# Kernel tuning notes

Measured on AMD Instinct MI355X. Metric: run time of the kernel, lower is better.

Reference implementation:

```python
import jax, jax.numpy as jnp
import numpy as np

N_NODES = 50000
N_EDGES = 800000
IN_FEATS = 128
OUT_FEATS = 128


def setup_inputs() -> dict:
    key = jax.random.key(0)
    k1, k2, k3, k4, k5 = jax.random.split(key, 5)
    feat = jax.random.normal(k1, (N_NODES, IN_FEATS), dtype=jnp.float32)
    src = jax.random.randint(k2, (N_EDGES,), 0, N_NODES, dtype=jnp.int64)
    dst = jax.random.randint(k3, (N_EDGES,), 0, N_NODES, dtype=jnp.int64)
    # Glorot uniform weight, zero bias (as in reset_parameters)
    limit = float(np.sqrt(6.0 / (IN_FEATS + OUT_FEATS)))
    weight = jax.random.uniform(k4, (IN_FEATS, OUT_FEATS), dtype=jnp.float32,
                                minval=-limit, maxval=limit)
    bias = jnp.zeros((OUT_FEATS,), dtype=jnp.float32)
    return {"feat": feat, "src": src, "dst": dst, "weight": weight, "bias": bias}


def reference(feat, src, dst, weight, bias):
    ones = jnp.ones(src.shape[0], dtype=feat.dtype)
    # out-degree normalization on source side
    deg_out = jnp.maximum(jax.ops.segment_sum(ones, src, num_segments=N_NODES), 1.0)
    h = feat * (deg_out ** -0.5)[:, None]  # [N, in]
    # in_feats <= out_feats: aggregate first, then matmul
    agg = jax.ops.segment_sum(h[src], dst, num_segments=N_NODES)  # SpMM: [N, in]
    rst = jnp.matmul(agg, weight)  # [N, out]
    # in-degree normalization on destination side
    deg_in = jnp.maximum(jax.ops.segment_sum(ones, dst, num_segments=N_NODES), 1.0)
    rst = rst * (deg_in ** -0.5)[:, None]
    rst = rst + bias
    return rst
```

## Files before the change

kernel.cpp:

```cpp
#include <hip/hip_runtime.h>

#define IN_F 128
#define HRH 4
#define HCD 64
#define HCS 32
#define HRB 16
#define HIST_RS 12544
#define BIN_RS 3136
#define LROW 68

typedef __attribute__((ext_vector_type(8))) short bf16x8;
typedef __attribute__((ext_vector_type(4))) float f32x4;

static __device__ __forceinline__ unsigned short f2bf(float x) {
    unsigned u = __float_as_uint(x);
    unsigned r = (u + 0x7FFFu + ((u >> 16) & 1u)) >> 16;
    return (unsigned short)r;
}

__global__ __launch_bounds__(256) void k_hist(const int* __restrict__ src,
                                              const int* __restrict__ dst,
                                              int* __restrict__ dstpart,
                                              int* __restrict__ srcpart,
                                              int nN, int nE) {
    __shared__ int h[HIST_RS];
    int bid = blockIdx.x;
    const int* key;
    int* part;
    int r, c, nch;
    if (bid < HRH * HCD) {
        key = dst; part = dstpart; nch = HCD;
        r = bid / HCD; c = bid % HCD;
    } else {
        bid -= HRH * HCD;
        key = src; part = srcpart; nch = HCS;
        r = bid / HCS; c = bid % HCS;
    }
    const int rs   = (nN + HRH - 1) / HRH;
    const int rbeg = r * rs;
    const int rsize = min(rs, nN - rbeg);
    if (rsize <= 0) return;

    for (int i = threadIdx.x; i < rsize; i += 256) h[i] = 0;
    __syncthreads();

    const int chunk = (nE + nch - 1) / nch;
    const int ebeg = c * chunk;
    const int eend = min(ebeg + chunk, nE);

    if ((ebeg & 3) == 0) {
        for (int i = ebeg + threadIdx.x * 4; i < eend; i += 256 * 4) {
            if (i + 3 < eend) {
                const int4 k4 = *reinterpret_cast<const int4*>(key + i);
                int a;
                a = k4.x - rbeg; if ((unsigned)a < (unsigned)rsize) atomicAdd(&h[a], 1);
                a = k4.y - rbeg; if ((unsigned)a < (unsigned)rsize) atomicAdd(&h[a], 1);
                a = k4.z - rbeg; if ((unsigned)a < (unsigned)rsize) atomicAdd(&h[a], 1);
                a = k4.w - rbeg; if ((unsigned)a < (unsigned)rsize) atomicAdd(&h[a], 1);
            } else {
                for (int j = i; j < eend; ++j) {
                    int a = key[j] - rbeg;
                    if ((unsigned)a < (unsigned)rsize) atomicAdd(&h[a], 1);
                }
            }
        }
    } else {
        for (int i = ebeg + threadIdx.x; i < eend; i += 256) {
            int a = key[i] - rbeg;
            if ((unsigned)a < (unsigned)rsize) atomicAdd(&h[a], 1);
        }
    }
    __syncthreads();

    int* pout = part + (size_t)c * nN + rbeg;
    for (int i = threadIdx.x; i < rsize; i += 256) pout[i] = h[i];
}

__global__ void k_merge(int* __restrict__ dstpart, const int* __restrict__ srcpart,
                        int* __restrict__ cnt_in,
                        float* __restrict__ dinv_out, float* __restrict__ dinv_in,
                        int nN) {
    const int n = blockIdx.x * blockDim.x + threadIdx.x;
    if (n >= nN) return;
    int s = 0;
#pragma unroll 4
    for (int c = 0; c < HCS; ++c) s += srcpart[(size_t)c * nN + n];
    int run = 0;
#pragma unroll 4
    for (int c = 0; c < HCD; ++c) {
        const size_t idx = (size_t)c * nN + n;
        int v = dstpart[idx];
        dstpart[idx] = run;
        run += v;
    }
    cnt_in[n]   = run;
    dinv_out[n] = rsqrtf(fmaxf((float)s, 1.0f));
    dinv_in[n]  = rsqrtf(fmaxf((float)run, 1.0f));
}

__global__ __launch_bounds__(256) void k_scan_blk(const int* __restrict__ cnt,
                                                  int* __restrict__ offs,
                                                  int* __restrict__ part, int nN) {
    __shared__ int ts[256];
    const int t = threadIdx.x;
    const int base = blockIdx.x * 1024 + t * 4;
    int4 v = make_int4(0, 0, 0, 0);
    if (base + 3 < nN) {
        v = *reinterpret_cast<const int4*>(cnt + base);
    } else {
        if (base + 0 < nN) v.x = cnt[base + 0];
        if (base + 1 < nN) v.y = cnt[base + 1];
        if (base + 2 < nN) v.z = cnt[base + 2];
        if (base + 3 < nN) v.w = cnt[base + 3];
    }
    const int s = v.x + v.y + v.z + v.w;
    ts[t] = s;
    __syncthreads();
    for (int d = 1; d < 256; d <<= 1) {
        int u = (t >= d) ? ts[t - d] : 0;
        __syncthreads();
        ts[t] += u;
        __syncthreads();
    }
    const int ex = ts[t] - s;
    if (t == 255) part[blockIdx.x] = ts[255];
    int4 o;
    o.x = ex;
    o.y = o.x + v.x;
    o.z = o.y + v.y;
    o.w = o.z + v.z;
    if (base + 3 < nN) {
        *reinterpret_cast<int4*>(offs + base) = o;
    } else {
        if (base + 0 < nN) offs[base + 0] = o.x;
        if (base + 1 < nN) offs[base + 1] = o.y;
        if (base + 2 < nN) offs[base + 2] = o.z;
        if (base + 3 < nN) offs[base + 3] = o.w;
    }
}

__global__ __launch_bounds__(256) void k_scan_top(int* __restrict__ part, int nb) {
    __shared__ int ts[256];
    const int t = threadIdx.x;
    const int v = (t < nb) ? part[t] : 0;
    ts[t] = v;
    __syncthreads();
    for (int d = 1; d < 256; d <<= 1) {
        int u = (t >= d) ? ts[t - d] : 0;
        __syncthreads();
        ts[t] += u;
        __syncthreads();
    }
    if (t < nb) part[t] = ts[t] - v;
}

__global__ __launch_bounds__(256) void k_scan_add(int* __restrict__ offs,
                                                  const int* __restrict__ part,
                                                  int nN, int nE) {
    const int base = blockIdx.x * 1024 + threadIdx.x * 4;
    const int add = part[blockIdx.x];
    if (base + 3 < nN) {
        int4 o = *reinterpret_cast<int4*>(offs + base);
        o.x += add; o.y += add; o.z += add; o.w += add;
        *reinterpret_cast<int4*>(offs + base) = o;
    } else {
#pragma unroll
        for (int j = 0; j < 4; ++j)
            if (base + j < nN) offs[base + j] += add;
    }
    if (blockIdx.x == 0 && threadIdx.x == 0) offs[nN] = nE;
}

__global__ __launch_bounds__(256) void k_bin2(const int* __restrict__ src,
                                              const int* __restrict__ dst,
                                              const int* __restrict__ offs,
                                              const int* __restrict__ chunkoff,
                                              int* __restrict__ eidx, int nN, int nE) {
    __shared__ int cur[BIN_RS];
    const int bid = blockIdx.x;
    const int r = bid / HCD;
    const int c = bid % HCD;
    const int rs = (nN + HRB - 1) / HRB;
    const int rbeg = r * rs;
    const int rsize = min(rs, nN - rbeg);
    if (rsize <= 0) return;

    for (int i = threadIdx.x; i < rsize; i += 256)
        cur[i] = offs[rbeg + i] + chunkoff[(size_t)c * nN + rbeg + i];
    __syncthreads();

    const int chunk = (nE + HCD - 1) / HCD;
    const int ebeg = c * chunk;
    const int eend = min(ebeg + chunk, nE);
    for (int i = ebeg + threadIdx.x * 4; i < eend; i += 256 * 4) {
        if (i + 3 < eend) {
            const int4 d4 = *reinterpret_cast<const int4*>(dst + i);
            int d;
            d = d4.x - rbeg; if ((unsigned)d < (unsigned)rsize) { int p = atomicAdd(&cur[d], 1); eidx[p] = src[i + 0]; }
            d = d4.y - rbeg; if ((unsigned)d < (unsigned)rsize) { int p = atomicAdd(&cur[d], 1); eidx[p] = src[i + 1]; }
            d = d4.z - rbeg; if ((unsigned)d < (unsigned)rsize) { int p = atomicAdd(&cur[d], 1); eidx[p] = src[i + 2]; }
            d = d4.w - rbeg; if ((unsigned)d < (unsigned)rsize) { int p = atomicAdd(&cur[d], 1); eidx[p] = src[i + 3]; }
        } else {
            for (int j = i; j < eend; ++j) {
                int d = dst[j] - rbeg;
                if ((unsigned)d < (unsigned)rsize) { int p = atomicAdd(&cur[d], 1); eidx[p] = src[j]; }
            }
        }
    }
}

__global__ __launch_bounds__(256) void k_scale(const float* __restrict__ feat,
                                               const float* __restrict__ dinv,
                                               unsigned short* __restrict__ h, int nN) {
    const int i = blockIdx.x * 256 + threadIdx.x;
    if (i >= nN * (IN_F / 4)) return;
    const int node = i >> 5;
    const int j = (i & 31) * 4;
    const float s = dinv[node];
    const float4 v = *reinterpret_cast<const float4*>(feat + (size_t)node * IN_F + j);
    ushort4 o;
    o.x = f2bf(v.x * s);
    o.y = f2bf(v.y * s);
    o.z = f2bf(v.z * s);
    o.w = f2bf(v.w * s);
    *reinterpret_cast<ushort4*>(h + (size_t)node * IN_F + j) = o;
}

__global__ __launch_bounds__(256) void k_wprep(const float* __restrict__ W,
                                               unsigned short* __restrict__ wt) {
    __shared__ float wl[128 * 128];
    for (int i = threadIdx.x * 4; i < 128 * 128; i += 256 * 4)
        *reinterpret_cast<float4*>(&wl[i]) = *reinterpret_cast<const float4*>(&W[i]);
    __syncthreads();
    const int col = threadIdx.x >> 1;
    const int k0  = (threadIdx.x & 1) * 64;
    for (int k = k0; k < k0 + 64; ++k)
        wt[col * 128 + k] = f2bf(wl[k * 128 + col]);
}

__global__ __launch_bounds__(256) void k_gg(
    const unsigned short* __restrict__ h, const int* __restrict__ eidx,
    const int* __restrict__ offs, const unsigned short* __restrict__ wt,
    const float* __restrict__ bias, const float* __restrict__ dinv_in,
    float* __restrict__ out, int nN) {
    __shared__ unsigned tile[16 * LROW];
    const int lane = threadIdx.x & 63;
    const int wave = threadIdx.x >> 6;
    const int blk16 = blockIdx.x * 16;
    const size_t lo = (size_t)(lane * 2);

    for (int j = 0; j < 4; ++j) {
        const int trow = wave * 4 + j;
        const int node = blk16 + trow;
        float ax = 0.0f, ay = 0.0f;
        if (node < nN) {
            const int beg = offs[node], end = offs[node + 1];
            int i = beg;
            for (; i + 8 <= end; i += 8) {
                const int s0 = eidx[i + 0], s1 = eidx[i + 1], s2 = eidx[i + 2], s3 = eidx[i + 3];
                const int s4 = eidx[i + 4], s5 = eidx[i + 5], s6 = eidx[i + 6], s7 = eidx[i + 7];
                const unsigned v0 = *reinterpret_cast<const unsigned*>(h + (size_t)s0 * IN_F + lo);
                const unsigned v1 = *reinterpret_cast<const unsigned*>(h + (size_t)s1 * IN_F + lo);
                const unsigned v2 = *reinterpret_cast<const unsigned*>(h + (size_t)s2 * IN_F + lo);
                const unsigned v3 = *reinterpret_cast<const unsigned*>(h + (size_t)s3 * IN_F + lo);
                const unsigned v4 = *reinterpret_cast<const unsigned*>(h + (size_t)s4 * IN_F + lo);
                const unsigned v5 = *reinterpret_cast<const unsigned*>(h + (size_t)s5 * IN_F + lo);
                const unsigned v6 = *reinterpret_cast<const unsigned*>(h + (size_t)s6 * IN_F + lo);
                const unsigned v7 = *reinterpret_cast<const unsigned*>(h + (size_t)s7 * IN_F + lo);
                ax += __uint_as_float(v0 << 16);          ay += __uint_as_float(v0 & 0xFFFF0000u);
                ax += __uint_as_float(v1 << 16);          ay += __uint_as_float(v1 & 0xFFFF0000u);
                ax += __uint_as_float(v2 << 16);          ay += __uint_as_float(v2 & 0xFFFF0000u);
                ax += __uint_as_float(v3 << 16);          ay += __uint_as_float(v3 & 0xFFFF0000u);
                ax += __uint_as_float(v4 << 16);          ay += __uint_as_float(v4 & 0xFFFF0000u);
                ax += __uint_as_float(v5 << 16);          ay += __uint_as_float(v5 & 0xFFFF0000u);
                ax += __uint_as_float(v6 << 16);          ay += __uint_as_float(v6 & 0xFFFF0000u);
                ax += __uint_as_float(v7 << 16);          ay += __uint_as_float(v7 & 0xFFFF0000u);
            }
            for (; i < end; ++i) {
                const int s = eidx[i];
                const unsigned v = *reinterpret_cast<const unsigned*>(h + (size_t)s * IN_F + lo);
                ax += __uint_as_float(v << 16);
                ay += __uint_as_float(v & 0xFFFF0000u);
            }
        }
        tile[trow * LROW + lane] = ((unsigned)f2bf(ay) << 16) | (unsigned)f2bf(ax);
    }
    __syncthreads();

    const int g = lane >> 4;
    const int cl = lane & 15;

    float di[4];
#pragma unroll
    for (int q = 0; q < 4; ++q)
        di[q] = dinv_in[min(blk16 + g * 4 + q, nN - 1)];

    f32x4 acc0 = (f32x4){0.f, 0.f, 0.f, 0.f};
    f32x4 acc1 = (f32x4){0.f, 0.f, 0.f, 0.f};
    const int col0 = wave * 16 + cl;
    const int col1 = (wave + 4) * 16 + cl;

#pragma unroll
    for (int s = 0; s < 4; ++s) {
        const bf16x8 a = *reinterpret_cast<const bf16x8*>(tile + cl * LROW + s * 16 + g * 4);
        const bf16x8 b0 = *reinterpret_cast<const bf16x8*>(wt + (size_t)col0 * IN_F + s * 32 + g * 8);
        const bf16x8 b1 = *reinterpret_cast<const bf16x8*>(wt + (size_t)col1 * IN_F + s * 32 + g * 8);
        acc0 = __builtin_amdgcn_mfma_f32_16x16x32_bf16(a, b0, acc0, 0, 0, 0);
        acc1 = __builtin_amdgcn_mfma_f32_16x16x32_bf16(a, b1, acc1, 0, 0, 0);
    }

    const float bv0 = bias[col0];
    const float bv1 = bias[col1];
#pragma unroll
    for (int q = 0; q < 4; ++q) {
        const int rr = blk16 + g * 4 + q;
        if (rr < nN) {
            out[(size_t)rr * IN_F + col0] = acc0[q] * di[q] + bv0;
            out[(size_t)rr * IN_F + col1] = acc1[q] * di[q] + bv1;
        }
    }
}

extern "C" void kernel_launch(void* const* d_in, const int* in_sizes, int n_in,
                              void* d_out, int out_size, void* d_ws, size_t ws_size,
                              hipStream_t stream) {
    const float* feat = (const float*)d_in[0];
    const int*   src  = (const int*)d_in[1];
    const int*   dst  = (const int*)d_in[2];
    const float* W    = (const float*)d_in[3];
    const float* bias = (const float*)d_in[4];
    float*       out  = (float*)d_out;

    const int nE = in_sizes[1];
    const int nN = in_sizes[0] / IN_F;
    const int nb = (nN + 1023) / 1024;

    char* base = (char*)d_ws;
    int*            dstpart  = (int*)base;
    int*            srcpart  = (int*)(base + (size_t)HCD * nN * 4);
    unsigned short* h        = (unsigned short*)base;
    int*            eidx     = (int*)(base + (size_t)HCD * nN * 4 + (size_t)nN * IN_F * 2);
    unsigned short* wt       = (unsigned short*)(eidx + nE);
    int*            cnt_in   = (int*)(wt + 128 * 128);
    float*          dinv_out = (float*)(cnt_in + nN);
    float*          dinv_in  = dinv_out + nN;
    int*            offs     = (int*)(dinv_in + nN);
    int*            partscan = offs + nN + 1;

    k_hist    <<<HRH * (HCD + HCS), 256, 0, stream>>>(src, dst, dstpart, srcpart, nN, nE);
    k_merge   <<<(nN + 255) / 256, 256, 0, stream>>>(dstpart, srcpart, cnt_in, dinv_out, dinv_in, nN);
    k_scan_blk<<<nb, 256, 0, stream>>>(cnt_in, offs, partscan, nN);
    k_scan_top<<<1, 256, 0, stream>>>(partscan, nb);
    k_scan_add<<<nb, 256, 0, stream>>>(offs, partscan, nN, nE);
    k_bin2    <<<HRB * HCD, 256, 0, stream>>>(src, dst, offs, dstpart, eidx, nN, nE);
    k_scale   <<<(nN * (IN_F / 4) + 255) / 256, 256, 0, stream>>>(feat, dinv_out, h, nN);
    k_wprep   <<<1, 256, 0, stream>>>(W, wt);
    k_gg      <<<(nN + 15) / 16, 256, 0, stream>>>(h, eidx, offs, wt, bias, dinv_in, out, nN);
}
```

Baseline: 132.4 us.

## Pad per-node edge lists to multiples of eight and halve bin row blocks

Measured after the change: 121.3 us. -8.4%, faster.

```diff
diff --git a/kernel.cpp b/kernel.cpp
--- a/kernel.cpp
+++ b/kernel.cpp
@@ -4,9 +4,9 @@
 #define HRH 4
 #define HCD 64
 #define HCS 32
-#define HRB 16
+#define HRB 8
 #define HIST_RS 12544
-#define BIN_RS 3136
+#define BIN_RS 6272
 #define LROW 68
 
 typedef __attribute__((ext_vector_type(8))) short bf16x8;
@@ -77,11 +77,12 @@
 }
 
 __global__ void k_merge(int* __restrict__ dstpart, const int* __restrict__ srcpart,
-                        int* __restrict__ cnt_in,
+                        int* __restrict__ cnt_pad, int* __restrict__ creal,
                         float* __restrict__ dinv_out, float* __restrict__ dinv_in,
                         int nN) {
     const int n = blockIdx.x * blockDim.x + threadIdx.x;
-    if (n >= nN) return;
+    if (n > nN) return;
+    if (n == nN) { cnt_pad[n] = 0; return; }
     int s = 0;
 #pragma unroll 4
     for (int c = 0; c < HCS; ++c) s += srcpart[(size_t)c * nN + n];
@@ -93,25 +94,26 @@
         dstpart[idx] = run;
         run += v;
     }
-    cnt_in[n]   = run;
+    cnt_pad[n]  = (run + 7) & ~7;
+    creal[n]    = run;
     dinv_out[n] = rsqrtf(fmaxf((float)s, 1.0f));
     dinv_in[n]  = rsqrtf(fmaxf((float)run, 1.0f));
 }
 
 __global__ __launch_bounds__(256) void k_scan_blk(const int* __restrict__ cnt,
                                                   int* __restrict__ offs,
-                                                  int* __restrict__ part, int nN) {
+                                                  int* __restrict__ part, int nNs) {
     __shared__ int ts[256];
     const int t = threadIdx.x;
     const int base = blockIdx.x * 1024 + t * 4;
     int4 v = make_int4(0, 0, 0, 0);
-    if (base + 3 < nN) {
+    if (base + 3 < nNs) {
         v = *reinterpret_cast<const int4*>(cnt + base);
     } else {
-        if (base + 0 < nN) v.x = cnt[base + 0];
-        if (base + 1 < nN) v.y = cnt[base + 1];
-        if (base + 2 < nN) v.z = cnt[base + 2];
-        if (base + 3 < nN) v.w = cnt[base + 3];
+        if (base + 0 < nNs) v.x = cnt[base + 0];
+        if (base + 1 < nNs) v.y = cnt[base + 1];
+        if (base + 2 < nNs) v.z = cnt[base + 2];
+        if (base + 3 < nNs) v.w = cnt[base + 3];
     }
     const int s = v.x + v.y + v.z + v.w;
     ts[t] = s;
@@ -129,13 +131,13 @@
     o.y = o.x + v.x;
     o.z = o.y + v.y;
     o.w = o.z + v.z;
-    if (base + 3 < nN) {
+    if (base + 3 < nNs) {
         *reinterpret_cast<int4*>(offs + base) = o;
     } else {
-        if (base + 0 < nN) offs[base + 0] = o.x;
-        if (base + 1 < nN) offs[base + 1] = o.y;
-        if (base + 2 < nN) offs[base + 2] = o.z;
-        if (base + 3 < nN) offs[base + 3] = o.w;
+        if (base + 0 < nNs) offs[base + 0] = o.x;
+        if (base + 1 < nNs) offs[base + 1] = o.y;
+        if (base + 2 < nNs) offs[base + 2] = o.z;
+        if (base + 3 < nNs) offs[base + 3] = o.w;
     }
 }
 
@@ -156,19 +158,27 @@
 
 __global__ __launch_bounds__(256) void k_scan_add(int* __restrict__ offs,
                                                   const int* __restrict__ part,
-                                                  int nN, int nE) {
+                                                  int nNs) {
     const int base = blockIdx.x * 1024 + threadIdx.x * 4;
     const int add = part[blockIdx.x];
-    if (base + 3 < nN) {
+    if (base + 3 < nNs) {
         int4 o = *reinterpret_cast<int4*>(offs + base);
         o.x += add; o.y += add; o.z += add; o.w += add;
         *reinterpret_cast<int4*>(offs + base) = o;
     } else {
 #pragma unroll
         for (int j = 0; j < 4; ++j)
-            if (base + j < nN) offs[base + j] += add;
-    }
-    if (blockIdx.x == 0 && threadIdx.x == 0) offs[nN] = nE;
+            if (base + j < nNs) offs[base + j] += add;
+    }
+}
+
+__global__ void k_pad(const int* __restrict__ offs, const int* __restrict__ creal,
+                      int* __restrict__ eidx, int nN) {
+    const int n = blockIdx.x * blockDim.x + threadIdx.x;
+    if (n >= nN) return;
+    const int s = offs[n] + creal[n];
+    const int e = offs[n + 1];
+    for (int i = s; i < e; ++i) eidx[i] = nN;
 }
 
 __global__ __launch_bounds__(256) void k_bin2(const int* __restrict__ src,
@@ -213,16 +223,18 @@
                                                const float* __restrict__ dinv,
                                                unsigned short* __restrict__ h, int nN) {
     const int i = blockIdx.x * 256 + threadIdx.x;
-    if (i >= nN * (IN_F / 4)) return;
+    if (i >= (nN + 1) * (IN_F / 4)) return;
     const int node = i >> 5;
     const int j = (i & 31) * 4;
-    const float s = dinv[node];
-    const float4 v = *reinterpret_cast<const float4*>(feat + (size_t)node * IN_F + j);
-    ushort4 o;
-    o.x = f2bf(v.x * s);
-    o.y = f2bf(v.y * s);
-    o.z = f2bf(v.z * s);
-    o.w = f2bf(v.w * s);
+    ushort4 o = make_ushort4(0, 0, 0, 0);
+    if (node < nN) {
+        const float s = dinv[node];
+        const float4 v = *reinterpret_cast<const float4*>(feat + (size_t)node * IN_F + j);
+        o.x = f2bf(v.x * s);
+        o.y = f2bf(v.y * s);
+        o.z = f2bf(v.z * s);
+        o.w = f2bf(v.w * s);
+    }
     *reinterpret_cast<ushort4*>(h + (size_t)node * IN_F + j) = o;
 }
 
@@ -255,32 +267,33 @@
         float ax = 0.0f, ay = 0.0f;
         if (node < nN) {
             const int beg = offs[node], end = offs[node + 1];
-            int i = beg;
-            for (; i + 8 <= end; i += 8) {
-                const int s0 = eidx[i + 0], s1 = eidx[i + 1], s2 = eidx[i + 2], s3 = eidx[i + 3];
-                const int s4 = eidx[i + 4], s5 = eidx[i + 5], s6 = eidx[i + 6], s7 = eidx[i + 7];
-                const unsigned v0 = *reinterpret_cast<const unsigned*>(h + (size_t)s0 * IN_F + lo);
-                const unsigned v1 = *reinterpret_cast<const unsigned*>(h + (size_t)s1 * IN_F + lo);
-                const unsigned v2 = *reinterpret_cast<const unsigned*>(h + (size_t)s2 * IN_F + lo);
-                const unsigned v3 = *reinterpret_cast<const unsigned*>(h + (size_t)s3 * IN_F + lo);
-                const unsigned v4 = *reinterpret_cast<const unsigned*>(h + (size_t)s4 * IN_F + lo);
-                const unsigned v5 = *reinterpret_cast<const unsigned*>(h + (size_t)s5 * IN_F + lo);
-                const unsigned v6 = *reinterpret_cast<const unsigned*>(h + (size_t)s6 * IN_F + lo);
-                const unsigned v7 = *reinterpret_cast<const unsigned*>(h + (size_t)s7 * IN_F + lo);
-                ax += __uint_as_float(v0 << 16);          ay += __uint_as_float(v0 & 0xFFFF0000u);
-                ax += __uint_as_float(v1 << 16);          ay += __uint_as_float(v1 & 0xFFFF0000u);
-                ax += __uint_as_float(v2 << 16);          ay += __uint_as_float(v2 & 0xFFFF0000u);
-                ax += __uint_as_float(v3 << 16);          ay += __uint_as_float(v3 & 0xFFFF0000u);
-                ax += __uint_as_float(v4 << 16);          ay += __uint_as_float(v4 & 0xFFFF0000u);
-                ax += __uint_as_float(v5 << 16);          ay += __uint_as_float(v5 & 0xFFFF0000u);
-                ax += __uint_as_float(v6 << 16);          ay += __uint_as_float(v6 & 0xFFFF0000u);
-                ax += __uint_as_float(v7 << 16);          ay += __uint_as_float(v7 & 0xFFFF0000u);
-            }
-            for (; i < end; ++i) {
-                const int s = eidx[i];
-                const unsigned v = *reinterpret_cast<const unsigned*>(h + (size_t)s * IN_F + lo);
-                ax += __uint_as_float(v << 16);
-                ay += __uint_as_float(v & 0xFFFF0000u);
+            if (beg < end) {
+                int4 ea = *reinterpret_cast<const int4*>(eidx + beg);
+                int4 eb = *reinterpret_cast<const int4*>(eidx + beg + 4);
+                for (int i = beg; i < end; i += 8) {
+                    const int s0 = ea.x, s1 = ea.y, s2 = ea.z, s3 = ea.w;
+                    const int s4 = eb.x, s5 = eb.y, s6 = eb.z, s7 = eb.w;
+                    const unsigned v0 = *reinterpret_cast<const unsigned*>(h + (size_t)s0 * IN_F + lo);
+                    const unsigned v1 = *reinterpret_cast<const unsigned*>(h + (size_t)s1 * IN_F + lo);
+                    const unsigned v2 = *reinterpret_cast<const unsigned*>(h + (size_t)s2 * IN_F + lo);
+                    const unsigned v3 = *reinterpret_cast<const unsigned*>(h + (size_t)s3 * IN_F + lo);
+                    const unsigned v4 = *reinterpret_cast<const unsigned*>(h + (size_t)s4 * IN_F + lo);
+                    const unsigned v5 = *reinterpret_cast<const unsigned*>(h + (size_t)s5 * IN_F + lo);
+                    const unsigned v6 = *reinterpret_cast<const unsigned*>(h + (size_t)s6 * IN_F + lo);
+                    const unsigned v7 = *reinterpret_cast<const unsigned*>(h + (size_t)s7 * IN_F + lo);
+                    if (i + 8 < end) {
+                        ea = *reinterpret_cast<const int4*>(eidx + i + 8);
+                        eb = *reinterpret_cast<const int4*>(eidx + i + 12);
+                    }
+                    ax += __uint_as_float(v0 << 16);          ay += __uint_as_float(v0 & 0xFFFF0000u);
+                    ax += __uint_as_float(v1 << 16);          ay += __uint_as_float(v1 & 0xFFFF0000u);
+                    ax += __uint_as_float(v2 << 16);          ay += __uint_as_float(v2 & 0xFFFF0000u);
+                    ax += __uint_as_float(v3 << 16);          ay += __uint_as_float(v3 & 0xFFFF0000u);
+                    ax += __uint_as_float(v4 << 16);          ay += __uint_as_float(v4 & 0xFFFF0000u);
+                    ax += __uint_as_float(v5 << 16);          ay += __uint_as_float(v5 & 0xFFFF0000u);
+                    ax += __uint_as_float(v6 << 16);          ay += __uint_as_float(v6 & 0xFFFF0000u);
+                    ax += __uint_as_float(v7 << 16);          ay += __uint_as_float(v7 & 0xFFFF0000u);
+                }
             }
         }
         tile[trow * LROW + lane] = ((unsigned)f2bf(ay) << 16) | (unsigned)f2bf(ax);
@@ -333,27 +346,31 @@
 
     const int nE = in_sizes[1];
     const int nN = in_sizes[0] / IN_F;
-    const int nb = (nN + 1023) / 1024;
+    const int nNs = nN + 1;
+    const int nb = (nNs + 1023) / 1024;
 
     char* base = (char*)d_ws;
     int*            dstpart  = (int*)base;
     int*            srcpart  = (int*)(base + (size_t)HCD * nN * 4);
     unsigned short* h        = (unsigned short*)base;
-    int*            eidx     = (int*)(base + (size_t)HCD * nN * 4 + (size_t)nN * IN_F * 2);
-    unsigned short* wt       = (unsigned short*)(eidx + nE);
-    int*            cnt_in   = (int*)(wt + 128 * 128);
-    float*          dinv_out = (float*)(cnt_in + nN);
+    int*            eidx     = (int*)(base + (size_t)(HCD + HCS) * nN * 4);
+    int*            eidx_end = eidx + nE + 8 * nN;
+    unsigned short* wt       = (unsigned short*)eidx_end;
+    int*            cnt_pad  = (int*)(wt + 128 * 128);
+    int*            creal    = cnt_pad + nNs + 4;
+    float*          dinv_out = (float*)(creal + nN + 4);
     float*          dinv_in  = dinv_out + nN;
     int*            offs     = (int*)(dinv_in + nN);
-    int*            partscan = offs + nN + 1;
+    int*            partscan = offs + nNs + 4;
 
     k_hist    <<<HRH * (HCD + HCS), 256, 0, stream>>>(src, dst, dstpart, srcpart, nN, nE);
-    k_merge   <<<(nN + 255) / 256, 256, 0, stream>>>(dstpart, srcpart, cnt_in, dinv_out, dinv_in, nN);
-    k_scan_blk<<<nb, 256, 0, stream>>>(cnt_in, offs, partscan, nN);
+    k_merge   <<<(nNs + 255) / 256, 256, 0, stream>>>(dstpart, srcpart, cnt_pad, creal, dinv_out, dinv_in, nN);
+    k_scan_blk<<<nb, 256, 0, stream>>>(cnt_pad, offs, partscan, nNs);
     k_scan_top<<<1, 256, 0, stream>>>(partscan, nb);
-    k_scan_add<<<nb, 256, 0, stream>>>(offs, partscan, nN, nE);
+    k_scan_add<<<nb, 256, 0, stream>>>(offs, partscan, nNs);
+    k_pad     <<<(nN + 255) / 256, 256, 0, stream>>>(offs, creal, eidx, nN);
     k_bin2    <<<HRB * HCD, 256, 0, stream>>>(src, dst, offs, dstpart, eidx, nN, nE);
-    k_scale   <<<(nN * (IN_F / 4) + 255) / 256, 256, 0, stream>>>(feat, dinv_out, h, nN);
+    k_scale   <<<((nN + 1) * (IN_F / 4) + 255) / 256, 256, 0, stream>>>(feat, dinv_out, h, nN);
     k_wprep   <<<1, 256, 0, stream>>>(W, wt);
     k_gg      <<<(nN + 15) / 16, 256, 0, stream>>>(h, eidx, offs, wt, bias, dinv_in, out, nN);
 }
```
